# Performance work log

Hardware: AMD Instinct MI355X
Metric: run time of the kernel (lower is better)

## Reference

```python
import jax, jax.numpy as jnp
import numpy as np

N = 100000      # nodes
E = 1600000     # edges
IN, H, OUT = 128, 128, 64
P_DROP = 0.5


def _glorot_linear(key, out_d, in_d):
    # PyG Linear default init (kaiming-uniform-ish); exact init is irrelevant for the baseline
    bound = 1.0 / np.sqrt(in_d)
    return jax.random.uniform(key, (out_d, in_d), jnp.float32, -bound, bound)


def setup_inputs() -> dict:
    key = jax.random.key(0)
    ks = jax.random.split(key, 8)
    x = jax.random.normal(ks[0], (N, IN), jnp.float32)
    edge_index = jax.random.randint(ks[1], (2, E), 0, N, dtype=jnp.int64)
    W1l = _glorot_linear(ks[2], H, IN)
    b1 = jnp.zeros((H,), jnp.float32)
    W1r = _glorot_linear(ks[3], H, IN)
    W2l = _glorot_linear(ks[4], OUT, H)
    b2 = jnp.zeros((OUT,), jnp.float32)
    W2r = _glorot_linear(ks[5], OUT, H)
    return dict(x=x, edge_index=edge_index, W1l=W1l, b1=b1, W1r=W1r,
                W2l=W2l, b2=b2, W2r=W2r)


def _sage_conv(x, src, dst, Wl, bl, Wr):
    # PyG SAGEConv (aggr='mean'): out = lin_l(mean_{j in N(i)} x_j) + lin_r(x_i)
    msg = x[src]                                             # [E, d] gather
    agg = jax.ops.segment_sum(msg, dst, num_segments=N)      # [N, d] scatter-add
    cnt = jax.ops.segment_sum(jnp.ones((src.shape[0], 1), x.dtype), dst,
                              num_segments=N)                # [N, 1] in-degree
    mean = agg / jnp.maximum(cnt, 1.0)                       # isolated nodes -> 0
    return mean @ Wl.T + bl + x @ Wr.T


def reference(x, edge_index, W1l, b1, W1r, W2l, b2, W2r):
    src, dst = edge_index[0], edge_index[1]
    h = _sage_conv(x, src, dst, W1l, b1, W1r)
    h = jax.nn.relu(h)
    # F.dropout(p=0.5) made deterministic with a fixed key
    keep = jax.random.bernoulli(jax.random.key(42), 1.0 - P_DROP, h.shape)
    h = jnp.where(keep, h / (1.0 - P_DROP), 0.0)
    return _sage_conv(h, src, dst, W2l, b2, W2r)
```

## Files before the change

### kernel.cpp

```cpp
#include <hip/hip_runtime.h>
#include <hip/hip_bf16.h>

#define N_NODES 100000
#define NE      1600000

#define BINSH 7
#define NBIN  782
#define BCAP  3072
#define SEPB  16384
#define NBLK  ((NE + SEPB - 1) / SEPB)
#define NMASKW 200000

typedef __attribute__((ext_vector_type(8))) short bfrag;
typedef __attribute__((ext_vector_type(4))) float ffrag;

#define BFLO(u) __uint_as_float((u) << 16)
#define BFHI(u) __uint_as_float((u) & 0xffff0000u)

__device__ __forceinline__ unsigned tf_rotl(unsigned x, int d) {
    return (x << d) | (x >> (32 - d));
}

__device__ __forceinline__ unsigned tf_word(unsigned f) {
    const unsigned ks0 = 0u;
    const unsigned ks1 = 42u;
    const unsigned ks2 = 0x1BD11BDAu ^ 0u ^ 42u;
    unsigned x0 = 0u + ks0;
    unsigned x1 = f + ks1;
#define TF_RND(r) { x0 += x1; x1 = tf_rotl(x1, r); x1 ^= x0; }
    TF_RND(13) TF_RND(15) TF_RND(26) TF_RND(6)
    x0 += ks1; x1 += ks2 + 1u;
    TF_RND(17) TF_RND(29) TF_RND(16) TF_RND(24)
    x0 += ks2; x1 += ks0 + 2u;
    TF_RND(13) TF_RND(15) TF_RND(26) TF_RND(6)
    x0 += ks0; x1 += ks1 + 3u;
    TF_RND(17) TF_RND(29) TF_RND(16) TF_RND(24)
    x0 += ks1; x1 += ks2 + 4u;
    TF_RND(13) TF_RND(15) TF_RND(26) TF_RND(6)
    x0 += ks2; x1 += ks0 + 5u;
#undef TF_RND
    return x0 ^ x1;
}

__device__ __forceinline__ unsigned short bf_bits(float v) {
    __hip_bfloat16 b = __float2bfloat16(v);
    return *(unsigned short*)&b;
}

__global__ void k_mask(unsigned long long* __restrict__ km) {
    const int lane = threadIdx.x & 63;
    const int w0 = (blockIdx.x * blockDim.x + threadIdx.x) >> 6;
    const int nw = (gridDim.x * blockDim.x) >> 6;
    for (int widx = w0; widx < NMASKW; widx += nw) {
        unsigned wv = tf_word((unsigned)widx * 64u + (unsigned)lane);
        unsigned long long keep = __ballot(!(wv & 0x80000000u));
        if (lane == 0) km[widx] = keep;
    }
}

__global__ void k_detect(const int* __restrict__ ei, int* __restrict__ flag) {
    __shared__ int nz;
    if (threadIdx.x == 0) nz = 0;
    __syncthreads();
    for (int i = threadIdx.x; i < 1024; i += blockDim.x)
        if (ei[2 * i + 1] != 0) atomicAdd(&nz, 1);
    __syncthreads();
    if (threadIdx.x == 0) *flag = (nz == 0) ? 1 : 0;
}

__global__ void k_conv(const float4* __restrict__ in, ushort4* __restrict__ out,
                       int n4) {
    int i = blockIdx.x * blockDim.x + threadIdx.x;
    if (i < n4) {
        float4 v = in[i];
        ushort4 o;
        o.x = bf_bits(v.x);
        o.y = bf_bits(v.y);
        o.z = bf_bits(v.z);
        o.w = bf_bits(v.w);
        out[i] = o;
    }
}

__global__ void k_wconv(const float* __restrict__ a, const float* __restrict__ b,
                        const float* __restrict__ c, const float* __restrict__ d,
                        __hip_bfloat16* __restrict__ o) {
    int i = blockIdx.x * blockDim.x + threadIdx.x;
    if (i < 16384)      o[i] = __float2bfloat16(a[i]);
    else if (i < 32768) o[i] = __float2bfloat16(b[i - 16384]);
    else if (i < 40960) o[i] = __float2bfloat16(c[i - 32768]);
    else if (i < 49152) o[i] = __float2bfloat16(d[i - 40960]);
}

__global__ __launch_bounds__(1024) void k_binscatter(const int* __restrict__ ei,
        const int* __restrict__ flag, int* __restrict__ bincur,
        int2* __restrict__ pairs) {
    __shared__ int h[NBIN];
    __shared__ int lbase[NBIN];
    for (int i = threadIdx.x; i < NBIN; i += 1024) h[i] = 0;
    __syncthreads();
    const int is64 = *flag;
    const int e0 = blockIdx.x * SEPB + threadIdx.x;
    int d[16], s[16];
#pragma unroll
    for (int k = 0; k < 16; ++k) {
        int e = e0 + k * 1024;
        if (e < NE) {
            d[k] = is64 ? ei[2 * (NE + e)] : ei[NE + e];
            s[k] = is64 ? ei[2 * e]        : ei[e];
            atomicAdd(&h[d[k] >> BINSH], 1);
        } else {
            d[k] = -1; s[k] = 0;
        }
    }
    __syncthreads();
    for (int i = threadIdx.x; i < NBIN; i += 1024) {
        int c = h[i];
        lbase[i] = c ? atomicAdd(&bincur[i], c) : 0;
        h[i] = 0;
    }
    __syncthreads();
#pragma unroll
    for (int k = 0; k < 16; ++k) {
        if (d[k] >= 0) {
            int b = d[k] >> BINSH;
            int r = atomicAdd(&h[b], 1);
            pairs[(size_t)b * BCAP + lbase[b] + r] = make_int2(s[k], d[k]);
        }
    }
}

__global__ __launch_bounds__(1024) void k_binscan(const int* __restrict__ bincnt,
        int* __restrict__ binptr) {
    __shared__ int sm[1024];
    const int t = threadIdx.x;
    int v = (t < NBIN) ? bincnt[t] : 0;
    sm[t] = v;
    __syncthreads();
    for (int off = 1; off < 1024; off <<= 1) {
        int u = (t >= off) ? sm[t - off] : 0;
        __syncthreads();
        sm[t] += u;
        __syncthreads();
    }
    if (t < NBIN) binptr[t] = sm[t] - v;
}

__global__ __launch_bounds__(256) void k_bin2csr(const int2* __restrict__ pairs,
        const int* __restrict__ binptr, const int* __restrict__ bincnt,
        int* __restrict__ ptr, int* __restrict__ adj) {
    __shared__ int cnt[128];
    __shared__ int sc[128];
    __shared__ int woff[128];
    const int b = blockIdx.x;
    const int base = binptr[b];
    const int nb = bincnt[b];
    const int2* pb = pairs + (size_t)b * BCAP;
    const int t = threadIdx.x;
    if (t < 128) cnt[t] = 0;
    __syncthreads();
    for (int i = t; i < nb; i += 256)
        atomicAdd(&cnt[pb[i].y & 127], 1);
    __syncthreads();
    if (t < 128) sc[t] = cnt[t];
    __syncthreads();
    for (int o = 1; o < 128; o <<= 1) {
        int u = 0;
        if (t < 128 && t >= o) u = sc[t - o];
        __syncthreads();
        if (t < 128) sc[t] += u;
        __syncthreads();
    }
    if (t < 128) {
        int ex = sc[t] - cnt[t];
        int node = b * 128 + t;
        if (node <= N_NODES) ptr[node] = base + ex;
        woff[t] = ex;
    }
    __syncthreads();
    for (int i = t; i < nb; i += 256) {
        int2 p = pb[i];
        int r = atomicAdd(&woff[p.y & 127], 1);
        adj[base + r] = p.x;
    }
}

__global__ void k_agg(const __hip_bfloat16* __restrict__ feat,
                      const int* __restrict__ ptr, const int* __restrict__ adj,
                      __hip_bfloat16* __restrict__ mean) {
    const int wid = (blockIdx.x * blockDim.x + threadIdx.x) >> 6;
    const int lane = threadIdx.x & 63;
    if (wid >= N_NODES) return;
    const int p0 = ptr[wid], p1 = ptr[wid + 1];
    float a0 = 0.f, b0 = 0.f, a1 = 0.f, b1 = 0.f;
    float a2 = 0.f, b2 = 0.f, a3 = 0.f, b3 = 0.f;
    int p = p0;
    for (; p + 7 < p1; p += 8) {
        int s0 = adj[p],     s1 = adj[p + 1], s2 = adj[p + 2], s3 = adj[p + 3];
        int s4 = adj[p + 4], s5 = adj[p + 5], s6 = adj[p + 6], s7 = adj[p + 7];
        unsigned u0 = *(const unsigned*)(feat + (size_t)s0 * 128 + lane * 2);
        unsigned u1 = *(const unsigned*)(feat + (size_t)s1 * 128 + lane * 2);
        unsigned u2 = *(const unsigned*)(feat + (size_t)s2 * 128 + lane * 2);
        unsigned u3 = *(const unsigned*)(feat + (size_t)s3 * 128 + lane * 2);
        unsigned u4 = *(const unsigned*)(feat + (size_t)s4 * 128 + lane * 2);
        unsigned u5 = *(const unsigned*)(feat + (size_t)s5 * 128 + lane * 2);
        unsigned u6 = *(const unsigned*)(feat + (size_t)s6 * 128 + lane * 2);
        unsigned u7 = *(const unsigned*)(feat + (size_t)s7 * 128 + lane * 2);
        a0 += BFLO(u0); b0 += BFHI(u0); a1 += BFLO(u1); b1 += BFHI(u1);
        a2 += BFLO(u2); b2 += BFHI(u2); a3 += BFLO(u3); b3 += BFHI(u3);
        a0 += BFLO(u4); b0 += BFHI(u4); a1 += BFLO(u5); b1 += BFHI(u5);
        a2 += BFLO(u6); b2 += BFHI(u6); a3 += BFLO(u7); b3 += BFHI(u7);
    }
    for (; p + 3 < p1; p += 4) {
        int s0 = adj[p], s1 = adj[p + 1], s2 = adj[p + 2], s3 = adj[p + 3];
        unsigned u0 = *(const unsigned*)(feat + (size_t)s0 * 128 + lane * 2);
        unsigned u1 = *(const unsigned*)(feat + (size_t)s1 * 128 + lane * 2);
        unsigned u2 = *(const unsigned*)(feat + (size_t)s2 * 128 + lane * 2);
        unsigned u3 = *(const unsigned*)(feat + (size_t)s3 * 128 + lane * 2);
        a0 += BFLO(u0); b0 += BFHI(u0); a1 += BFLO(u1); b1 += BFHI(u1);
        a2 += BFLO(u2); b2 += BFHI(u2); a3 += BFLO(u3); b3 += BFHI(u3);
    }
    for (; p < p1; ++p) {
        int s0 = adj[p];
        unsigned u0 = *(const unsigned*)(feat + (size_t)s0 * 128 + lane * 2);
        a0 += BFLO(u0); b0 += BFHI(u0);
    }
    const float inv = 1.0f / (float)max(p1 - p0, 1);
    float m0 = ((a0 + a1) + (a2 + a3)) * inv;
    float m1 = ((b0 + b1) + (b2 + b3)) * inv;
    unsigned o = ((unsigned)bf_bits(m1) << 16) | (unsigned)bf_bits(m0);
    *(unsigned*)(mean + (size_t)wid * 128 + lane * 2) = o;
}

__global__ __launch_bounds__(256) void k_lin1f(
    const __hip_bfloat16* __restrict__ Am, const __hip_bfloat16* __restrict__ Ax,
    const __hip_bfloat16* __restrict__ W1l, const __hip_bfloat16* __restrict__ W1r,
    const float* __restrict__ b1,
    const __hip_bfloat16* __restrict__ W2l, const __hip_bfloat16* __restrict__ W2r,
    const float* __restrict__ b2,
    const unsigned long long* __restrict__ kmask,
    __hip_bfloat16* __restrict__ y2, float* __restrict__ zout) {
    __shared__ __align__(16) __hip_bfloat16 hs[64][136];
    const int tid = threadIdx.x;
    const int w  = tid >> 6;
    const int l  = tid & 63;
    const int lr = l & 15;
    const int lk = l >> 4;
    const int j0 = w * 32;
    const int j2 = w * 16 + lr;
    const int n0 = blockIdx.x * 64;

    bfrag B1[2][2][4];
#pragma unroll
    for (int jt = 0; jt < 2; ++jt) {
        const int jrow = j0 + jt * 16 + lr;
#pragma unroll
        for (int ks = 0; ks < 4; ++ks) {
            B1[jt][0][ks] = *(const bfrag*)(W1l + jrow * 128 + ks * 32 + lk * 8);
            B1[jt][1][ks] = *(const bfrag*)(W1r + jrow * 128 + ks * 32 + lk * 8);
        }
    }
    bfrag Bl2[4], Br2[4];
#pragma unroll
    for (int ks = 0; ks < 4; ++ks) {
        Bl2[ks] = *(const bfrag*)(W2l + j2 * 128 + ks * 32 + lk * 8);
        Br2[ks] = *(const bfrag*)(W2r + j2 * 128 + ks * 32 + lk * 8);
    }
    const float bj0 = b1[j0 + lr];
    const float bj1 = b1[j0 + 16 + lr];
    const float bj2 = b2[j2];

    for (int t = 0; t < 4; ++t) {
        const int rbase = n0 + t * 16;
        int arow = rbase + lr;
        if (arow > N_NODES - 1) arow = N_NODES - 1;
        ffrag acc0 = {0.f, 0.f, 0.f, 0.f};
        ffrag acc1 = {0.f, 0.f, 0.f, 0.f};
#pragma unroll
        for (int ks = 0; ks < 4; ++ks) {
            bfrag am = *(const bfrag*)(Am + (size_t)arow * 128 + ks * 32 + lk * 8);
            bfrag ax = *(const bfrag*)(Ax + (size_t)arow * 128 + ks * 32 + lk * 8);
            acc0 = __builtin_amdgcn_mfma_f32_16x16x32_bf16(am, B1[0][0][ks], acc0, 0, 0, 0);
            acc1 = __builtin_amdgcn_mfma_f32_16x16x32_bf16(am, B1[1][0][ks], acc1, 0, 0, 0);
            acc0 = __builtin_amdgcn_mfma_f32_16x16x32_bf16(ax, B1[0][1][ks], acc0, 0, 0, 0);
            acc1 = __builtin_amdgcn_mfma_f32_16x16x32_bf16(ax, B1[1][1][ks], acc1, 0, 0, 0);
        }
#pragma unroll
        for (int r = 0; r < 4; ++r) {
            const int n = rbase + lk * 4 + r;
            const int lrow = t * 16 + lk * 4 + r;
            const int nm = (n < N_NODES) ? n : (N_NODES - 1);
            const unsigned long long km = kmask[nm * 2 + (j0 >> 6)];
            float v0 = fmaxf(acc0[r] + bj0, 0.f);
            v0 = ((km >> ((j0 + lr) & 63)) & 1ull) ? (v0 + v0) : 0.f;
            hs[lrow][j0 + lr] = __float2bfloat16(v0);
            float v1 = fmaxf(acc1[r] + bj1, 0.f);
            v1 = ((km >> ((j0 + 16 + lr) & 63)) & 1ull) ? (v1 + v1) : 0.f;
            hs[lrow][j0 + 16 + lr] = __float2bfloat16(v1);
        }
    }
    __syncthreads();

    for (int t = 0; t < 4; ++t) {
        ffrag accY = {0.f, 0.f, 0.f, 0.f};
        ffrag accZ = {0.f, 0.f, 0.f, 0.f};
#pragma unroll
        for (int ks = 0; ks < 4; ++ks) {
            bfrag ah = *(const bfrag*)&hs[t * 16 + lr][ks * 32 + lk * 8];
            accY = __builtin_amdgcn_mfma_f32_16x16x32_bf16(ah, Bl2[ks], accY, 0, 0, 0);
            accZ = __builtin_amdgcn_mfma_f32_16x16x32_bf16(ah, Br2[ks], accZ, 0, 0, 0);
        }
#pragma unroll
        for (int r = 0; r < 4; ++r) {
            const int n = n0 + t * 16 + lk * 4 + r;
            if (n < N_NODES) {
                y2[(size_t)n * 64 + j2]   = __float2bfloat16(accY[r]);
                zout[(size_t)n * 64 + j2] = accZ[r] + bj2;
            }
        }
    }
}

__global__ void k_agg2f(const __hip_bfloat16* __restrict__ feat,
                        const int* __restrict__ ptr, const int* __restrict__ adj,
                        float* __restrict__ out) {
    const int node = (blockIdx.x * blockDim.x + threadIdx.x) >> 5;
    const int sl = threadIdx.x & 31;
    if (node >= N_NODES) return;
    const int p0 = ptr[node], p1 = ptr[node + 1];
    float a0 = 0.f, b0 = 0.f, a1 = 0.f, b1 = 0.f;
    float a2 = 0.f, b2 = 0.f, a3 = 0.f, b3 = 0.f;
    int p = p0;
    for (; p + 7 < p1; p += 8) {
        int s0 = adj[p],     s1 = adj[p + 1], s2 = adj[p + 2], s3 = adj[p + 3];
        int s4 = adj[p + 4], s5 = adj[p + 5], s6 = adj[p + 6], s7 = adj[p + 7];
        unsigned u0 = *(const unsigned*)(feat + (size_t)s0 * 64 + sl * 2);
        unsigned u1 = *(const unsigned*)(feat + (size_t)s1 * 64 + sl * 2);
        unsigned u2 = *(const unsigned*)(feat + (size_t)s2 * 64 + sl * 2);
        unsigned u3 = *(const unsigned*)(feat + (size_t)s3 * 64 + sl * 2);
        unsigned u4 = *(const unsigned*)(feat + (size_t)s4 * 64 + sl * 2);
        unsigned u5 = *(const unsigned*)(feat + (size_t)s5 * 64 + sl * 2);
        unsigned u6 = *(const unsigned*)(feat + (size_t)s6 * 64 + sl * 2);
        unsigned u7 = *(const unsigned*)(feat + (size_t)s7 * 64 + sl * 2);
        a0 += BFLO(u0); b0 += BFHI(u0); a1 += BFLO(u1); b1 += BFHI(u1);
        a2 += BFLO(u2); b2 += BFHI(u2); a3 += BFLO(u3); b3 += BFHI(u3);
        a0 += BFLO(u4); b0 += BFHI(u4); a1 += BFLO(u5); b1 += BFHI(u5);
        a2 += BFLO(u6); b2 += BFHI(u6); a3 += BFLO(u7); b3 += BFHI(u7);
    }
    for (; p + 3 < p1; p += 4) {
        int s0 = adj[p], s1 = adj[p + 1], s2 = adj[p + 2], s3 = adj[p + 3];
        unsigned u0 = *(const unsigned*)(feat + (size_t)s0 * 64 + sl * 2);
        unsigned u1 = *(const unsigned*)(feat + (size_t)s1 * 64 + sl * 2);
        unsigned u2 = *(const unsigned*)(feat + (size_t)s2 * 64 + sl * 2);
        unsigned u3 = *(const unsigned*)(feat + (size_t)s3 * 64 + sl * 2);
        a0 += BFLO(u0); b0 += BFHI(u0); a1 += BFLO(u1); b1 += BFHI(u1);
        a2 += BFLO(u2); b2 += BFHI(u2); a3 += BFLO(u3); b3 += BFHI(u3);
    }
    for (; p < p1; ++p) {
        int s0 = adj[p];
        unsigned u0 = *(const unsigned*)(feat + (size_t)s0 * 64 + sl * 2);
        a0 += BFLO(u0); b0 += BFHI(u0);
    }
    const float inv = 1.0f / (float)max(p1 - p0, 1);
    float m0 = ((a0 + a1) + (a2 + a3)) * inv;
    float m1 = ((b0 + b1) + (b2 + b3)) * inv;
    float2 z = *(const float2*)(out + (size_t)node * 64 + sl * 2);
    float2 o;
    o.x = z.x + m0;
    o.y = z.y + m1;
    *(float2*)(out + (size_t)node * 64 + sl * 2) = o;
}

extern "C" void kernel_launch(void* const* d_in, const int* in_sizes, int n_in,
                              void* d_out, int out_size, void* d_ws, size_t ws_size,
                              hipStream_t stream) {
    const float* x   = (const float*)d_in[0];
    const int*   ei  = (const int*)d_in[1];
    const float* W1l = (const float*)d_in[2];
    const float* b1  = (const float*)d_in[3];
    const float* W1r = (const float*)d_in[4];
    const float* W2l = (const float*)d_in[5];
    const float* b2  = (const float*)d_in[6];
    const float* W2r = (const float*)d_in[7];
    float* out = (float*)d_out;

    char* w = (char*)d_ws;
    int* flag   = (int*)w;
    int* bincur = flag + 64;
    int* binptr = bincur + 1024;
    int* ptr    = binptr + 1024;
    int* adj    = ptr + (N_NODES + 1);
    size_t koff = (((size_t)(64 + 1024 + 1024 + N_NODES + 1 + NE)) * 4 + 255)
                  & ~(size_t)255;
    unsigned long long* kmask = (unsigned long long*)(w + koff);
    size_t foff = (koff + (size_t)NMASKW * 8 + 255) & ~(size_t)255;
    __hip_bfloat16* wb    = (__hip_bfloat16*)(w + foff);
    __hip_bfloat16* w1lb  = wb;
    __hip_bfloat16* w1rb  = wb + 16384;
    __hip_bfloat16* w2lb  = wb + 32768;
    __hip_bfloat16* w2rb  = wb + 40960;
    __hip_bfloat16* xb    = wb + 49152;
    __hip_bfloat16* meanb = xb + (size_t)N_NODES * 128;
    char* pregion = (char*)(meanb + (size_t)N_NODES * 128);
    int2* pairs = (int2*)pregion;
    __hip_bfloat16* y2b = (__hip_bfloat16*)pregion;

    hipMemsetAsync(bincur, 0, 1024 * sizeof(int), stream);

    const int n4 = N_NODES * 128 / 4;
    k_conv<<<(n4 + 255) / 256, 256, 0, stream>>>((const float4*)x, (ushort4*)xb, n4);
    k_wconv<<<192, 256, 0, stream>>>(W1l, W1r, W2l, W2r, wb);
    k_detect<<<1, 256, 0, stream>>>(ei, flag);
    k_mask<<<1024, 256, 0, stream>>>(kmask);

    k_binscatter<<<NBLK, 1024, 0, stream>>>(ei, flag, bincur, pairs);
    k_binscan<<<1, 1024, 0, stream>>>(bincur, binptr);
    k_bin2csr<<<NBIN, 256, 0, stream>>>(pairs, binptr, bincur, ptr, adj);

    const int ab  = (N_NODES + 3) / 4;
    const int nb  = (N_NODES + 63) / 64;
    const int ab2 = (N_NODES + 7) / 8;

    k_agg<<<ab, 256, 0, stream>>>(xb, ptr, adj, meanb);
    k_lin1f<<<nb, 256, 0, stream>>>(meanb, xb, w1lb, w1rb, b1,
                                    w2lb, w2rb, b2, kmask, y2b, out);
    k_agg2f<<<ab2, 256, 0, stream>>>(y2b, ptr, adj, out);
}
```

Baseline: 249.3 us.

## Pack edge pairs, drop binscan and memset, widen aggregation gathers

Edge pairs are packed into one 32-bit word (local dst in the high bits, src in the low 17 bits), which halves the scatter and CSR-build traffic. The separate bin scan kernel is removed: each bin2csr block computes its own base by reducing the preceding bin counts. The bincur memset moves into k_detect, which saves a launch. Both aggregation kernels now split the wave into two halves that handle alternating edges with 8-byte gathers and combine through a shuffle, so fewer, wider memory requests are issued per neighbour row.

```diff
diff --git a/kernel.cpp b/kernel.cpp
--- a/kernel.cpp
+++ b/kernel.cpp
@@ -58,12 +58,15 @@
     }
 }
 
-__global__ void k_detect(const int* __restrict__ ei, int* __restrict__ flag) {
+__global__ void k_detect(const int* __restrict__ ei, int* __restrict__ flag,
+                         int* __restrict__ bincur) {
     __shared__ int nz;
     if (threadIdx.x == 0) nz = 0;
     __syncthreads();
-    for (int i = threadIdx.x; i < 1024; i += blockDim.x)
+    for (int i = threadIdx.x; i < 1024; i += blockDim.x) {
         if (ei[2 * i + 1] != 0) atomicAdd(&nz, 1);
+        bincur[i] = 0;
+    }
     __syncthreads();
     if (threadIdx.x == 0) *flag = (nz == 0) ? 1 : 0;
 }
@@ -94,7 +97,7 @@
 
 __global__ __launch_bounds__(1024) void k_binscatter(const int* __restrict__ ei,
         const int* __restrict__ flag, int* __restrict__ bincur,
-        int2* __restrict__ pairs) {
+        int* __restrict__ pairs) {
     __shared__ int h[NBIN];
     __shared__ int lbase[NBIN];
     for (int i = threadIdx.x; i < NBIN; i += 1024) h[i] = 0;
@@ -125,42 +128,36 @@
         if (d[k] >= 0) {
             int b = d[k] >> BINSH;
             int r = atomicAdd(&h[b], 1);
-            pairs[(size_t)b * BCAP + lbase[b] + r] = make_int2(s[k], d[k]);
-        }
-    }
-}
-
-__global__ __launch_bounds__(1024) void k_binscan(const int* __restrict__ bincnt,
-        int* __restrict__ binptr) {
-    __shared__ int sm[1024];
-    const int t = threadIdx.x;
-    int v = (t < NBIN) ? bincnt[t] : 0;
-    sm[t] = v;
-    __syncthreads();
-    for (int off = 1; off < 1024; off <<= 1) {
-        int u = (t >= off) ? sm[t - off] : 0;
-        __syncthreads();
-        sm[t] += u;
-        __syncthreads();
-    }
-    if (t < NBIN) binptr[t] = sm[t] - v;
-}
-
-__global__ __launch_bounds__(256) void k_bin2csr(const int2* __restrict__ pairs,
-        const int* __restrict__ binptr, const int* __restrict__ bincnt,
-        int* __restrict__ ptr, int* __restrict__ adj) {
+            pairs[(size_t)b * BCAP + lbase[b] + r] =
+                ((d[k] & 127) << 17) | s[k];
+        }
+    }
+}
+
+__global__ __launch_bounds__(256) void k_bin2csr(const int* __restrict__ pairs,
+        const int* __restrict__ bincnt, int* __restrict__ ptr,
+        int* __restrict__ adj) {
+    __shared__ int red[256];
     __shared__ int cnt[128];
     __shared__ int sc[128];
     __shared__ int woff[128];
     const int b = blockIdx.x;
-    const int base = binptr[b];
+    const int t = threadIdx.x;
+    int s = 0;
+    for (int i = t; i < b; i += 256) s += bincnt[i];
+    red[t] = s;
+    __syncthreads();
+    for (int o = 128; o > 0; o >>= 1) {
+        if (t < o) red[t] += red[t + o];
+        __syncthreads();
+    }
+    const int base = red[0];
     const int nb = bincnt[b];
-    const int2* pb = pairs + (size_t)b * BCAP;
-    const int t = threadIdx.x;
+    const int* pb = pairs + (size_t)b * BCAP;
     if (t < 128) cnt[t] = 0;
     __syncthreads();
     for (int i = t; i < nb; i += 256)
-        atomicAdd(&cnt[pb[i].y & 127], 1);
+        atomicAdd(&cnt[(pb[i] >> 17) & 127], 1);
     __syncthreads();
     if (t < 128) sc[t] = cnt[t];
     __syncthreads();
@@ -179,9 +176,9 @@
     }
     __syncthreads();
     for (int i = t; i < nb; i += 256) {
-        int2 p = pb[i];
-        int r = atomicAdd(&woff[p.y & 127], 1);
-        adj[base + r] = p.x;
+        int pk = pb[i];
+        int r = atomicAdd(&woff[(pk >> 17) & 127], 1);
+        adj[base + r] = pk & 0x1FFFF;
     }
 }
 
@@ -192,44 +189,55 @@
     const int lane = threadIdx.x & 63;
     if (wid >= N_NODES) return;
     const int p0 = ptr[wid], p1 = ptr[wid + 1];
-    float a0 = 0.f, b0 = 0.f, a1 = 0.f, b1 = 0.f;
-    float a2 = 0.f, b2 = 0.f, a3 = 0.f, b3 = 0.f;
+    const int half = lane >> 5;
+    const size_t coff = (size_t)(lane & 31) * 4;
+    float c0 = 0.f, c1 = 0.f, c2 = 0.f, c3 = 0.f;
+    float d0 = 0.f, d1 = 0.f, d2 = 0.f, d3 = 0.f;
     int p = p0;
+    for (; p + 15 < p1; p += 16) {
+        int s[8];
+#pragma unroll
+        for (int k = 0; k < 8; ++k) s[k] = adj[p + 2 * k + half];
+#pragma unroll
+        for (int k = 0; k < 8; ++k) {
+            uint2 u = *(const uint2*)(feat + (size_t)s[k] * 128 + coff);
+            if (k & 1) { d0 += BFLO(u.x); d1 += BFHI(u.x); d2 += BFLO(u.y); d3 += BFHI(u.y); }
+            else       { c0 += BFLO(u.x); c1 += BFHI(u.x); c2 += BFLO(u.y); c3 += BFHI(u.y); }
+        }
+    }
     for (; p + 7 < p1; p += 8) {
-        int s0 = adj[p],     s1 = adj[p + 1], s2 = adj[p + 2], s3 = adj[p + 3];
-        int s4 = adj[p + 4], s5 = adj[p + 5], s6 = adj[p + 6], s7 = adj[p + 7];
-        unsigned u0 = *(const unsigned*)(feat + (size_t)s0 * 128 + lane * 2);
-        unsigned u1 = *(const unsigned*)(feat + (size_t)s1 * 128 + lane * 2);
-        unsigned u2 = *(const unsigned*)(feat + (size_t)s2 * 128 + lane * 2);
-        unsigned u3 = *(const unsigned*)(feat + (size_t)s3 * 128 + lane * 2);
-        unsigned u4 = *(const unsigned*)(feat + (size_t)s4 * 128 + lane * 2);
-        unsigned u5 = *(const unsigned*)(feat + (size_t)s5 * 128 + lane * 2);
-        unsigned u6 = *(const unsigned*)(feat + (size_t)s6 * 128 + lane * 2);
-        unsigned u7 = *(const unsigned*)(feat + (size_t)s7 * 128 + lane * 2);
-        a0 += BFLO(u0); b0 += BFHI(u0); a1 += BFLO(u1); b1 += BFHI(u1);
-        a2 += BFLO(u2); b2 += BFHI(u2); a3 += BFLO(u3); b3 += BFHI(u3);
-        a0 += BFLO(u4); b0 += BFHI(u4); a1 += BFLO(u5); b1 += BFHI(u5);
-        a2 += BFLO(u6); b2 += BFHI(u6); a3 += BFLO(u7); b3 += BFHI(u7);
-    }
-    for (; p + 3 < p1; p += 4) {
-        int s0 = adj[p], s1 = adj[p + 1], s2 = adj[p + 2], s3 = adj[p + 3];
-        unsigned u0 = *(const unsigned*)(feat + (size_t)s0 * 128 + lane * 2);
-        unsigned u1 = *(const unsigned*)(feat + (size_t)s1 * 128 + lane * 2);
-        unsigned u2 = *(const unsigned*)(feat + (size_t)s2 * 128 + lane * 2);
-        unsigned u3 = *(const unsigned*)(feat + (size_t)s3 * 128 + lane * 2);
-        a0 += BFLO(u0); b0 += BFHI(u0); a1 += BFLO(u1); b1 += BFHI(u1);
-        a2 += BFLO(u2); b2 += BFHI(u2); a3 += BFLO(u3); b3 += BFHI(u3);
-    }
-    for (; p < p1; ++p) {
-        int s0 = adj[p];
-        unsigned u0 = *(const unsigned*)(feat + (size_t)s0 * 128 + lane * 2);
-        a0 += BFLO(u0); b0 += BFHI(u0);
-    }
-    const float inv = 1.0f / (float)max(p1 - p0, 1);
-    float m0 = ((a0 + a1) + (a2 + a3)) * inv;
-    float m1 = ((b0 + b1) + (b2 + b3)) * inv;
-    unsigned o = ((unsigned)bf_bits(m1) << 16) | (unsigned)bf_bits(m0);
-    *(unsigned*)(mean + (size_t)wid * 128 + lane * 2) = o;
+        int s[4];
+#pragma unroll
+        for (int k = 0; k < 4; ++k) s[k] = adj[p + 2 * k + half];
+#pragma unroll
+        for (int k = 0; k < 4; ++k) {
+            uint2 u = *(const uint2*)(feat + (size_t)s[k] * 128 + coff);
+            if (k & 1) { d0 += BFLO(u.x); d1 += BFHI(u.x); d2 += BFLO(u.y); d3 += BFHI(u.y); }
+            else       { c0 += BFLO(u.x); c1 += BFHI(u.x); c2 += BFLO(u.y); c3 += BFHI(u.y); }
+        }
+    }
+    for (; p + 1 < p1; p += 2) {
+        int s = adj[p + half];
+        uint2 u = *(const uint2*)(feat + (size_t)s * 128 + coff);
+        c0 += BFLO(u.x); c1 += BFHI(u.x); c2 += BFLO(u.y); c3 += BFHI(u.y);
+    }
+    if (p < p1 && half == 0) {
+        int s = adj[p];
+        uint2 u = *(const uint2*)(feat + (size_t)s * 128 + coff);
+        c0 += BFLO(u.x); c1 += BFHI(u.x); c2 += BFLO(u.y); c3 += BFHI(u.y);
+    }
+    c0 += d0; c1 += d1; c2 += d2; c3 += d3;
+    c0 += __shfl_xor(c0, 32);
+    c1 += __shfl_xor(c1, 32);
+    c2 += __shfl_xor(c2, 32);
+    c3 += __shfl_xor(c3, 32);
+    if (half == 0) {
+        const float inv = 1.0f / (float)max(p1 - p0, 1);
+        uint2 o;
+        o.x = ((unsigned)bf_bits(c1 * inv) << 16) | (unsigned)bf_bits(c0 * inv);
+        o.y = ((unsigned)bf_bits(c3 * inv) << 16) | (unsigned)bf_bits(c2 * inv);
+        *(uint2*)(mean + (size_t)wid * 128 + coff) = o;
+    }
 }
 
 __global__ __launch_bounds__(256) void k_lin1f(
@@ -328,47 +336,57 @@
     const int sl = threadIdx.x & 31;
     if (node >= N_NODES) return;
     const int p0 = ptr[node], p1 = ptr[node + 1];
-    float a0 = 0.f, b0 = 0.f, a1 = 0.f, b1 = 0.f;
-    float a2 = 0.f, b2 = 0.f, a3 = 0.f, b3 = 0.f;
+    const int sub = sl >> 4;
+    const size_t coff = (size_t)(sl & 15) * 4;
+    float c0 = 0.f, c1 = 0.f, c2 = 0.f, c3 = 0.f;
+    float d0 = 0.f, d1 = 0.f, d2 = 0.f, d3 = 0.f;
     int p = p0;
+    for (; p + 15 < p1; p += 16) {
+        int s[8];
+#pragma unroll
+        for (int k = 0; k < 8; ++k) s[k] = adj[p + 2 * k + sub];
+#pragma unroll
+        for (int k = 0; k < 8; ++k) {
+            uint2 u = *(const uint2*)(feat + (size_t)s[k] * 64 + coff);
+            if (k & 1) { d0 += BFLO(u.x); d1 += BFHI(u.x); d2 += BFLO(u.y); d3 += BFHI(u.y); }
+            else       { c0 += BFLO(u.x); c1 += BFHI(u.x); c2 += BFLO(u.y); c3 += BFHI(u.y); }
+        }
+    }
     for (; p + 7 < p1; p += 8) {
-        int s0 = adj[p],     s1 = adj[p + 1], s2 = adj[p + 2], s3 = adj[p + 3];
-        int s4 = adj[p + 4], s5 = adj[p + 5], s6 = adj[p + 6], s7 = adj[p + 7];
-        unsigned u0 = *(const unsigned*)(feat + (size_t)s0 * 64 + sl * 2);
-        unsigned u1 = *(const unsigned*)(feat + (size_t)s1 * 64 + sl * 2);
-        unsigned u2 = *(const unsigned*)(feat + (size_t)s2 * 64 + sl * 2);
-        unsigned u3 = *(const unsigned*)(feat + (size_t)s3 * 64 + sl * 2);
-        unsigned u4 = *(const unsigned*)(feat + (size_t)s4 * 64 + sl * 2);
-        unsigned u5 = *(const unsigned*)(feat + (size_t)s5 * 64 + sl * 2);
-        unsigned u6 = *(const unsigned*)(feat + (size_t)s6 * 64 + sl * 2);
-        unsigned u7 = *(const unsigned*)(feat + (size_t)s7 * 64 + sl * 2);
-        a0 += BFLO(u0); b0 += BFHI(u0); a1 += BFLO(u1); b1 += BFHI(u1);
-        a2 += BFLO(u2); b2 += BFHI(u2); a3 += BFLO(u3); b3 += BFHI(u3);
-        a0 += BFLO(u4); b0 += BFHI(u4); a1 += BFLO(u5); b1 += BFHI(u5);
-        a2 += BFLO(u6); b2 += BFHI(u6); a3 += BFLO(u7); b3 += BFHI(u7);
-    }
-    for (; p + 3 < p1; p += 4) {
-        int s0 = adj[p], s1 = adj[p + 1], s2 = adj[p + 2], s3 = adj[p + 3];
-        unsigned u0 = *(const unsigned*)(feat + (size_t)s0 * 64 + sl * 2);
-        unsigned u1 = *(const unsigned*)(feat + (size_t)s1 * 64 + sl * 2);
-        unsigned u2 = *(const unsigned*)(feat + (size_t)s2 * 64 + sl * 2);
-        unsigned u3 = *(const unsigned*)(feat + (size_t)s3 * 64 + sl * 2);
-        a0 += BFLO(u0); b0 += BFHI(u0); a1 += BFLO(u1); b1 += BFHI(u1);
-        a2 += BFLO(u2); b2 += BFHI(u2); a3 += BFLO(u3); b3 += BFHI(u3);
-    }
-    for (; p < p1; ++p) {
-        int s0 = adj[p];
-        unsigned u0 = *(const unsigned*)(feat + (size_t)s0 * 64 + sl * 2);
-        a0 += BFLO(u0); b0 += BFHI(u0);
-    }
-    const float inv = 1.0f / (float)max(p1 - p0, 1);
-    float m0 = ((a0 + a1) + (a2 + a3)) * inv;
-    float m1 = ((b0 + b1) + (b2 + b3)) * inv;
-    float2 z = *(const float2*)(out + (size_t)node * 64 + sl * 2);
-    float2 o;
-    o.x = z.x + m0;
-    o.y = z.y + m1;
-    *(float2*)(out + (size_t)node * 64 + sl * 2) = o;
+        int s[4];
+#pragma unroll
+        for (int k = 0; k < 4; ++k) s[k] = adj[p + 2 * k + sub];
+#pragma unroll
+        for (int k = 0; k < 4; ++k) {
+            uint2 u = *(const uint2*)(feat + (size_t)s[k] * 64 + coff);
+            if (k & 1) { d0 += BFLO(u.x); d1 += BFHI(u.x); d2 += BFLO(u.y); d3 += BFHI(u.y); }
+            else       { c0 += BFLO(u.x); c1 += BFHI(u.x); c2 += BFLO(u.y); c3 += BFHI(u.y); }
+        }
+    }
+    for (; p + 1 < p1; p += 2) {
+        int s = adj[p + sub];
+        uint2 u = *(const uint2*)(feat + (size_t)s * 64 + coff);
+        c0 += BFLO(u.x); c1 += BFHI(u.x); c2 += BFLO(u.y); c3 += BFHI(u.y);
+    }
+    if (p < p1 && sub == 0) {
+        int s = adj[p];
+        uint2 u = *(const uint2*)(feat + (size_t)s * 64 + coff);
+        c0 += BFLO(u.x); c1 += BFHI(u.x); c2 += BFLO(u.y); c3 += BFHI(u.y);
+    }
+    c0 += d0; c1 += d1; c2 += d2; c3 += d3;
+    c0 += __shfl_xor(c0, 16);
+    c1 += __shfl_xor(c1, 16);
+    c2 += __shfl_xor(c2, 16);
+    c3 += __shfl_xor(c3, 16);
+    if (sub == 0) {
+        const float inv = 1.0f / (float)max(p1 - p0, 1);
+        float4 z = *(const float4*)(out + (size_t)node * 64 + coff);
+        z.x += c0 * inv;
+        z.y += c1 * inv;
+        z.z += c2 * inv;
+        z.w += c3 * inv;
+        *(float4*)(out + (size_t)node * 64 + coff) = z;
+    }
 }
 
 extern "C" void kernel_launch(void* const* d_in, const int* in_sizes, int n_in,
@@ -387,10 +405,9 @@
     char* w = (char*)d_ws;
     int* flag   = (int*)w;
     int* bincur = flag + 64;
-    int* binptr = bincur + 1024;
-    int* ptr    = binptr + 1024;
+    int* ptr    = bincur + 1024;
     int* adj    = ptr + (N_NODES + 1);
-    size_t koff = (((size_t)(64 + 1024 + 1024 + N_NODES + 1 + NE)) * 4 + 255)
+    size_t koff = (((size_t)(64 + 1024 + N_NODES + 1 + NE)) * 4 + 255)
                   & ~(size_t)255;
     unsigned long long* kmask = (unsigned long long*)(w + koff);
     size_t foff = (koff + (size_t)NMASKW * 8 + 255) & ~(size_t)255;
@@ -402,20 +419,17 @@
     __hip_bfloat16* xb    = wb + 49152;
     __hip_bfloat16* meanb = xb + (size_t)N_NODES * 128;
     char* pregion = (char*)(meanb + (size_t)N_NODES * 128);
-    int2* pairs = (int2*)pregion;
+    int* pairs = (int*)pregion;
     __hip_bfloat16* y2b = (__hip_bfloat16*)pregion;
-
-    hipMemsetAsync(bincur, 0, 1024 * sizeof(int), stream);
 
     const int n4 = N_NODES * 128 / 4;
     k_conv<<<(n4 + 255) / 256, 256, 0, stream>>>((const float4*)x, (ushort4*)xb, n4);
     k_wconv<<<192, 256, 0, stream>>>(W1l, W1r, W2l, W2r, wb);
-    k_detect<<<1, 256, 0, stream>>>(ei, flag);
+    k_detect<<<1, 256, 0, stream>>>(ei, flag, bincur);
     k_mask<<<1024, 256, 0, stream>>>(kmask);
 
     k_binscatter<<<NBLK, 1024, 0, stream>>>(ei, flag, bincur, pairs);
-    k_binscan<<<1, 1024, 0, stream>>>(bincur, binptr);
-    k_bin2csr<<<NBIN, 256, 0, stream>>>(pairs, binptr, bincur, ptr, adj);
+    k_bin2csr<<<NBIN, 256, 0, stream>>>(pairs, bincur, ptr, adj);
 
     const int ab  = (N_NODES + 3) / 4;
     const int nb  = (N_NODES + 63) / 64;
```

Result: faster. 243.2 us (-2.4%).
